# Kernel tuning notes

Hardware: AMD Instinct MI355X
Metric: run time of the kernel (lower is better)

The kernel has to match this reference:

```python
import jax, jax.numpy as jnp
import numpy as np

N_NODES, N_EDGES, N_FEAT, N_HID = 50000, 800000, 512, 64


def gcn_conv(x, W, b, src, dst, ew):
    """PyG-style GCNConv: linear -> symmetric-normalized aggregation with self-loops -> +bias."""
    N = x.shape[0]
    h = x @ W  # [N, H]
    # degree includes the implicit self-loop of weight 1 (PyG gcn_norm default)
    deg = jax.ops.segment_sum(ew, dst, num_segments=N) + 1.0
    dinv = jax.lax.rsqrt(deg)  # deg^{-1/2}
    coef = dinv[src] * ew * dinv[dst]  # [E]
    out = jax.ops.segment_sum(h[src] * coef[:, None], dst, num_segments=N)
    out = out + h * (dinv * dinv)[:, None]  # self-loop contribution
    return out + b


def setup_inputs() -> dict:
    key = jax.random.key(0)
    k0, k1, k2, k3 = jax.random.split(key, 4)
    x = jax.random.normal(k0, (N_NODES, N_FEAT), dtype=jnp.float32)
    edge_index = jax.random.randint(k1, (2, N_EDGES), 0, N_NODES, dtype=jnp.int64)
    edge_weight = jnp.ones((N_EDGES,), dtype=jnp.float32)
    W1 = jax.random.normal(k2, (N_FEAT, N_HID), dtype=jnp.float32) * (1.0 / np.sqrt(N_FEAT))
    b1 = jnp.zeros((N_HID,), dtype=jnp.float32)
    W2 = jax.random.normal(k3, (N_HID, N_HID), dtype=jnp.float32) * (1.0 / np.sqrt(N_HID))
    b2 = jnp.zeros((N_HID,), dtype=jnp.float32)
    return {"x": x, "edge_index": edge_index, "edge_weight": edge_weight,
            "W1": W1, "b1": b1, "W2": W2, "b2": b2}


def reference(x, edge_index, edge_weight, W1, b1, W2, b2):
    # Grace.forward -> GCN_body.forward in eval mode (no dropout, no LN)
    src, dst = edge_index[0], edge_index[1]
    h = jax.nn.relu(gcn_conv(x, W1, b1, src, dst, edge_weight))
    h = jax.nn.relu(gcn_conv(h, W2, b2, src, dst, edge_weight))
    return h
```

## Files before the change

kernel.cpp:

```cpp
#include <hip/hip_runtime.h>
#include <hip/hip_bf16.h>

typedef __bf16 bf16x8 __attribute__((ext_vector_type(8)));
typedef float  f32x4  __attribute__((ext_vector_type(4)));

#define RNODES 64
#define ROWCAP 1792
#define NB 128
#define MAXNR 1024

__device__ __forceinline__ float bf_lo(unsigned int v) { return __uint_as_float(v << 16); }
__device__ __forceinline__ float bf_hi(unsigned int v) { return __uint_as_float(v & 0xFFFF0000u); }

__global__ void probe_kernel(const unsigned int* __restrict__ ew_raw,
                             const unsigned int* __restrict__ ei_raw,
                             int* __restrict__ flags) {
    if (blockIdx.x == 0 && threadIdx.x == 0) {
        flags[0] = (ew_raw[0] == 0x3F803F80u) ? 1 : 0;
        flags[1] = ((ei_raw[1] | ei_raw[3] | ei_raw[5] | ei_raw[7]) == 0u) ? 1 : 0;
        flags[2] = 0;
        flags[3] = 0;
        flags[4] = 1;
    }
}

__global__ void ones_kernel(const unsigned int* __restrict__ ew_raw,
                            int* __restrict__ flags, int E) {
    int f16 = flags[0];
    int nw = f16 ? (E >> 1) : E;
    unsigned int expect = f16 ? 0x3F803F80u : 0x3F800000u;
    int base = blockIdx.x * 1024 + threadIdx.x;
    unsigned int bad = 0;
    #pragma unroll
    for (int k = 0; k < 4; ++k) {
        int i = base + k * 256;
        if (i < nw) bad |= (ew_raw[i] ^ expect);
    }
    if (bad) flags[4] = 0;
}

__global__ void pack_kernel(const void* __restrict__ W, const int* __restrict__ flags,
                            __hip_bfloat16* __restrict__ Wp, int K) {
    int t = blockIdx.x * blockDim.x + threadIdx.x;
    if (t >= K * 64) return;
    int j  = t & 7;
    int l  = (t >> 3) & 63;
    int nt = (t >> 9) & 3;
    int kt = t >> 11;
    int k = kt * 32 + (l >> 4) * 8 + j;
    int n = nt * 16 + (l & 15);
    size_t gi = (size_t)k * 64 + n;
    if (flags[0]) Wp[t] = ((const __hip_bfloat16*)W)[gi];
    else          Wp[t] = __float2bfloat16(((const float*)W)[gi]);
}

__device__ __forceinline__ void gemm_body(const void* __restrict__ A,
                                          const __hip_bfloat16* __restrict__ Wp,
                                          int a_f32, __hip_bfloat16* __restrict__ out,
                                          int M, int K, int gt) {
    int wid  = gt >> 6;
    int lane = gt & 63;
    if (wid >= (M >> 4)) return;
    int row0 = wid << 4;
    int quad = lane >> 4, mr = lane & 15;

    const bf16x8* bp = (const bf16x8*)((const void*)Wp) + lane;

    f32x4 acc[4];
    #pragma unroll
    for (int nt = 0; nt < 4; ++nt) acc[nt] = (f32x4){0.f, 0.f, 0.f, 0.f};

    int KT = K >> 5;
    const __hip_bfloat16* ab   = (const __hip_bfloat16*)A + (size_t)(row0 + mr) * K + quad * 8;
    const float*          af32 = (const float*)A + (size_t)(row0 + mr) * K + quad * 8;

    for (int kt = 0; kt < KT; ++kt) {
        bf16x8 af;
        if (a_f32) {
            const float* ar = af32 + kt * 32;
            #pragma unroll
            for (int j = 0; j < 8; ++j) af[j] = (__bf16)ar[j];
        } else {
            af = ((const bf16x8*)((const void*)(ab + kt * 32)))[0];
        }
        #pragma unroll
        for (int nt = 0; nt < 4; ++nt) {
            bf16x8 bf = bp[(kt * 4 + nt) * 64];
            acc[nt] = __builtin_amdgcn_mfma_f32_16x16x32_bf16(af, bf, acc[nt], 0, 0, 0);
        }
    }

    __hip_bfloat16* o = out + (size_t)row0 * 64;
    #pragma unroll
    for (int nt = 0; nt < 4; ++nt)
        #pragma unroll
        for (int r = 0; r < 4; ++r)
            o[(size_t)(quad * 4 + r) * 64 + nt * 16 + mr] = __float2bfloat16(acc[nt][r]);
}

__global__ void gemm_mfma(const void* __restrict__ A, const __hip_bfloat16* __restrict__ Wp,
                          const int* __restrict__ flags, __hip_bfloat16* __restrict__ out,
                          int M, int K, int a_mode) {
    int gt = blockIdx.x * blockDim.x + threadIdx.x;
    int a_f32 = (a_mode == 2) && (flags[0] == 0);
    gemm_body(A, Wp, a_f32, out, M, K, gt);
}

__global__ void p1_kernel(const int* __restrict__ ei, const void* __restrict__ ew,
                          const int* __restrict__ flags,
                          int* __restrict__ blockhist, unsigned int* __restrict__ pkstage,
                          float* __restrict__ wstage, int E, int NR) {
    __shared__ int hist[MAXNR];
    int b = blockIdx.x, tid = threadIdx.x;
    for (int i = tid; i < NR; i += 256) hist[i] = 0;
    __syncthreads();
    int chunk = (E + NB - 1) / NB;
    int e0 = b * chunk;
    int e1 = e0 + chunk; if (e1 > E) e1 = E;
    int f16 = flags[0], i64 = flags[1], ones = flags[4];
    for (int e = e0 + tid; e < e1; e += 256) {
        int s, d;
        if (i64) { s = ei[2LL * e]; d = ei[2LL * ((long long)E + e)]; }
        else     { s = ei[e];       d = ei[E + e]; }
        int r = d >> 6;
        atomicAdd(&hist[r], 1);
        pkstage[e] = ((unsigned int)r << 22) | ((unsigned int)s << 6) | (unsigned int)(d & 63);
        if (!ones) {
            float w = f16 ? __bfloat162float(((const __hip_bfloat16*)ew)[e])
                          : ((const float*)ew)[e];
            wstage[e] = w;
        }
    }
    __syncthreads();
    for (int i = tid; i < NR; i += 256) blockhist[b * NR + i] = hist[i];
}

__global__ void p2_kernel(int* __restrict__ blockhist, int* __restrict__ rtot, int NR) {
    int r = blockIdx.x * blockDim.x + threadIdx.x;
    if (r >= NR) return;
    int run = r * ROWCAP;
    #pragma unroll 4
    for (int b = 0; b < NB; ++b) {
        int c = blockhist[b * NR + r];
        blockhist[b * NR + r] = run;
        run += c;
    }
    int tot = run - r * ROWCAP;
    rtot[r] = tot > ROWCAP ? ROWCAP : tot;
}

__global__ void p3_kernel(const int* __restrict__ blockhist,
                          const unsigned int* __restrict__ pkstage,
                          const float* __restrict__ wstage, const int* __restrict__ flags,
                          unsigned int* __restrict__ sortedR, float* __restrict__ sortedRW,
                          int E, int NR) {
    __shared__ int loff[MAXNR];
    int b = blockIdx.x, tid = threadIdx.x;
    for (int i = tid; i < NR; i += 256) loff[i] = blockhist[b * NR + i];
    __syncthreads();
    int chunk = (E + NB - 1) / NB;
    int e0 = b * chunk;
    int e1 = e0 + chunk; if (e1 > E) e1 = E;
    int ones = flags[4];
    for (int e = e0 + tid; e < e1; e += 256) {
        unsigned int pk = pkstage[e];
        int r = (int)(pk >> 22);
        int pos = atomicAdd(&loff[r], 1);
        if (pos < (r + 1) * ROWCAP) {
            sortedR[pos] = pk;
            if (!ones) sortedRW[pos] = wstage[e];
        }
    }
}

__global__ void range_kernel(const unsigned int* __restrict__ sortedR,
                             const float* __restrict__ sortedRW,
                             const int* __restrict__ rtot, const int* __restrict__ flags,
                             int* __restrict__ cnt, float* __restrict__ dinv,
                             int* __restrict__ row_ptr,
                             int* __restrict__ sortedS, float* __restrict__ sortedW, int N) {
    __shared__ unsigned int sd[ROWCAP];
    __shared__ float sw[ROWCAP];
    __shared__ int   cnt0[RNODES], pref[RNODES], slot[RNODES];
    __shared__ float wsum[RNODES];

    int r   = blockIdx.x;
    int tid = threadIdx.x;
    int ones = flags[4];
    int T = rtot[r];

    if (tid < RNODES) { cnt0[tid] = 0; wsum[tid] = 0.f; }
    __syncthreads();

    size_t g = (size_t)r * ROWCAP;
    for (int t = tid; t < T; t += 256) {
        sd[t] = sortedR[g + t];
        if (!ones) sw[t] = sortedRW[g + t];
    }
    __syncthreads();

    for (int k = tid; k < T; k += 256) {
        int dl = sd[k] & (RNODES - 1);
        atomicAdd(&cnt0[dl], 1);
        if (!ones) atomicAdd(&wsum[dl], sw[k]);
    }
    __syncthreads();

    if (tid < RNODES) pref[tid] = cnt0[tid];
    __syncthreads();
    for (int off = 1; off < RNODES; off <<= 1) {
        int v = (tid < RNODES && tid >= off) ? pref[tid - off] : 0;
        __syncthreads();
        if (tid < RNODES) pref[tid] += v;
        __syncthreads();
    }
    if (tid < RNODES) {
        int excl = pref[tid] - cnt0[tid];
        int n = r * RNODES + tid;
        slot[tid] = r * ROWCAP + excl;
        if (n < N) {
            cnt[n]     = cnt0[tid];
            row_ptr[n] = r * ROWCAP + excl;
            float wd = ones ? (float)cnt0[tid] : wsum[tid];
            dinv[n]  = rsqrtf(wd + 1.0f);
        }
    }
    __syncthreads();

    for (int k = tid; k < T; k += 256) {
        unsigned int v = sd[k];
        int dl = v & (RNODES - 1);
        int p = atomicAdd(&slot[dl], 1);
        sortedS[p] = (int)((v >> 6) & 0xFFFFu);
        if (!ones) sortedW[p] = sw[k];
    }
}

__global__ void check_fast(const void* __restrict__ A, const void* __restrict__ W,
                           int* __restrict__ flags, const __hip_bfloat16* __restrict__ out,
                           int N, int K, int a_mode, int fidx) {
    __shared__ float xs[4 * 512];
    int f16 = flags[0];
    int a_f32 = (a_mode == 2) && (f16 == 0);
    int tid = threadIdx.x;
    int total = 4 * K;
    for (int t = tid; t < total; t += 256) {
        int nn = t / K, kk = t - nn * K;
        int n = (int)(((long long)(blockIdx.x * 4 + nn) * 977) % N);
        long long gi = (long long)n * K + kk;
        float v = a_f32 ? (float)(__bf16)(((const float*)A)[gi])
                        : __bfloat162float(((const __hip_bfloat16*)A)[gi]);
        xs[t] = v;
    }
    __syncthreads();
    int j = tid & 63, local = tid >> 6;
    int n = (int)(((long long)(blockIdx.x * 4 + local) * 977) % N);
    const float* xr = xs + local * K;
    float acc = 0.f;
    if (f16) {
        const __hip_bfloat16* Wb = (const __hip_bfloat16*)W;
        #pragma unroll 8
        for (int k = 0; k < K; ++k) acc += xr[k] * __bfloat162float(Wb[(long long)k * 64 + j]);
    } else {
        const float* Wf = (const float*)W;
        #pragma unroll 8
        for (int k = 0; k < K; ++k) acc += xr[k] * (float)(__bf16)(Wf[(long long)k * 64 + j]);
    }
    float d = __bfloat162float(out[(size_t)n * 64 + j]) - acc;
    if (!(fabsf(d) <= 0.05f)) atomicAdd(&flags[fidx], 1);
}

__global__ void gemm_fix(const void* __restrict__ A, const void* __restrict__ W,
                         const int* __restrict__ flags, __hip_bfloat16* __restrict__ out,
                         int N, int K, int a_mode, int fidx) {
    if (flags[fidx] == 0) return;
    __shared__ float xs[4 * 512];
    int node0 = blockIdx.x * 4;
    int tid = threadIdx.x;
    int f16 = flags[0];
    int a_f32 = (a_mode == 2) && (f16 == 0);
    int total = 4 * K;
    for (int t = tid; t < total; t += 256) {
        int nn = t / K, kk = t - nn * K;
        long long gi = (long long)(node0 + nn) * K + kk;
        float v = a_f32 ? ((const float*)A)[gi]
                        : __bfloat162float(((const __hip_bfloat16*)A)[gi]);
        xs[t] = v;
    }
    __syncthreads();
    int j = tid & 63, local = tid >> 6;
    int n = node0 + local;
    if (n >= N) return;
    const float* xr = xs + local * K;
    float acc = 0.f;
    if (f16) {
        const __hip_bfloat16* Wb = (const __hip_bfloat16*)W;
        #pragma unroll 8
        for (int k = 0; k < K; ++k) acc += xr[k] * __bfloat162float(Wb[(long long)k * 64 + j]);
    } else {
        const float* Wf = (const float*)W;
        #pragma unroll 8
        for (int k = 0; k < K; ++k) acc += xr[k] * Wf[(long long)k * 64 + j];
    }
    out[(long long)n * 64 + j] = __float2bfloat16(acc);
}

__global__ void gather_kernel(const __hip_bfloat16* __restrict__ h,
                              const int* __restrict__ sortedS, const float* __restrict__ sortedW,
                              const int* __restrict__ cnt, const int* __restrict__ row_ptr,
                              const float* __restrict__ dinv,
                              const void* __restrict__ bias, const int* __restrict__ flags,
                              void* __restrict__ out, int internal, int N) {
    int gt = blockIdx.x * blockDim.x + threadIdx.x;
    int n = gt >> 5, jl = gt & 31;
    if (n >= N) return;
    int f16 = flags[0], ones = flags[4];
    float dn = dinv[n];
    int deg = cnt[n];
    int base = row_ptr[n];
    const int*   p  = sortedS + base;
    const float* pw = sortedW + base;
    const unsigned int* h32 = (const unsigned int*)h;
    float a0 = 0.f, a1 = 0.f;
    int s = 0;
    for (; s + 4 <= deg; s += 4) {
        int s0 = p[s], s1 = p[s + 1], s2 = p[s + 2], s3 = p[s + 3];
        float c0 = dinv[s0] * dn, c1 = dinv[s1] * dn;
        float c2 = dinv[s2] * dn, c3 = dinv[s3] * dn;
        if (!ones) { c0 *= pw[s]; c1 *= pw[s + 1]; c2 *= pw[s + 2]; c3 *= pw[s + 3]; }
        unsigned int v0 = h32[(size_t)s0 * 32 + jl];
        unsigned int v1 = h32[(size_t)s1 * 32 + jl];
        unsigned int v2 = h32[(size_t)s2 * 32 + jl];
        unsigned int v3 = h32[(size_t)s3 * 32 + jl];
        a0 += c0 * bf_lo(v0) + c1 * bf_lo(v1) + c2 * bf_lo(v2) + c3 * bf_lo(v3);
        a1 += c0 * bf_hi(v0) + c1 * bf_hi(v1) + c2 * bf_hi(v2) + c3 * bf_hi(v3);
    }
    for (; s < deg; ++s) {
        int s0 = p[s];
        float c = dinv[s0] * dn;
        if (!ones) c *= pw[s];
        unsigned int v = h32[(size_t)s0 * 32 + jl];
        a0 += c * bf_lo(v);
        a1 += c * bf_hi(v);
    }
    unsigned int vs = h32[(size_t)n * 32 + jl];
    float dn2 = dn * dn;
    a0 += dn2 * bf_lo(vs);
    a1 += dn2 * bf_hi(vs);
    if (f16) {
        unsigned int bv = ((const unsigned int*)bias)[jl];
        a0 += bf_lo(bv);
        a1 += bf_hi(bv);
    } else {
        a0 += ((const float*)bias)[jl * 2];
        a1 += ((const float*)bias)[jl * 2 + 1];
    }
    a0 = fmaxf(a0, 0.f);
    a1 = fmaxf(a1, 0.f);
    if (internal | f16) {
        __hip_bfloat16 b0 = __float2bfloat16(a0), b1 = __float2bfloat16(a1);
        unsigned int pack = ((unsigned int)(*(unsigned short*)&b1) << 16)
                          | (unsigned int)(*(unsigned short*)&b0);
        ((unsigned int*)out)[(size_t)n * 32 + jl] = pack;
    } else {
        ((float*)out)[(size_t)n * 64 + jl * 2]     = a0;
        ((float*)out)[(size_t)n * 64 + jl * 2 + 1] = a1;
    }
}

extern "C" void kernel_launch(void* const* d_in, const int* in_sizes, int n_in,
                              void* d_out, int out_size, void* d_ws, size_t ws_size,
                              hipStream_t stream) {
    const void* x  = d_in[0];
    const int*  ei = (const int*)d_in[1];
    const void* ew = d_in[2];
    const void* W1 = d_in[3];
    const void* b1 = d_in[4];
    const void* W2 = d_in[5];
    const void* b2 = d_in[6];

    const int H = in_sizes[4];
    const int F = in_sizes[3] / H;
    const int N = in_sizes[0] / F;
    const int E = in_sizes[1] / 2;

    const int NR = (N + RNODES - 1) / RNODES;

    char* w = (char*)d_ws;
    size_t off = 0;
    auto alloc = [&](size_t bytes) {
        char* r = w + off;
        off += (bytes + 255) & ~(size_t)255;
        return r;
    };
    int*   flags     = (int*)alloc(32);
    int*   blockhist = (int*)alloc((size_t)NB * NR * 4);
    int*   rtot      = (int*)alloc((size_t)NR * 4);
    int*   cnt       = (int*)alloc((size_t)N * 4);
    float* dinv      = (float*)alloc((size_t)N * 4);
    int*   row_ptr   = (int*)alloc((size_t)N * 4);
    unsigned int* pkstage = (unsigned int*)alloc((size_t)E * 4);
    float* wstage    = (float*)alloc((size_t)E * 4);
    unsigned int* sortedR = (unsigned int*)alloc((size_t)NR * ROWCAP * 4);
    float* sortedRW  = (float*)alloc((size_t)NR * ROWCAP * 4);
    int*   sortedS   = (int*)alloc((size_t)NR * ROWCAP * 4);
    float* sortedW   = (float*)alloc((size_t)NR * ROWCAP * 4);
    __hip_bfloat16* bufH = (__hip_bfloat16*)alloc((size_t)N * 64 * 2);
    __hip_bfloat16* bufR = (__hip_bfloat16*)alloc((size_t)N * 64 * 2);
    __hip_bfloat16* W1p  = (__hip_bfloat16*)alloc((size_t)F * 64 * 2);
    __hip_bfloat16* W2p  = (__hip_bfloat16*)alloc((size_t)H * 64 * 2);

    probe_kernel<<<1, 64, 0, stream>>>((const unsigned int*)ew, (const unsigned int*)ei, flags);
    ones_kernel<<<(E + 1023) / 1024, 256, 0, stream>>>((const unsigned int*)ew, flags, E);
    pack_kernel<<<(F * 64 + 255) / 256, 256, 0, stream>>>(W1, flags, W1p, F);
    pack_kernel<<<(H * 64 + 255) / 256, 256, 0, stream>>>(W2, flags, W2p, H);

    int gblocks = ((N / 16) * 64 + 255) / 256;

    p1_kernel<<<NB, 256, 0, stream>>>(ei, ew, flags, blockhist, pkstage, wstage, E, NR);
    p2_kernel<<<(NR + 255) / 256, 256, 0, stream>>>(blockhist, rtot, NR);
    p3_kernel<<<NB, 256, 0, stream>>>(blockhist, pkstage, wstage, flags,
                                      sortedR, sortedRW, E, NR);

    gemm_mfma<<<gblocks, 256, 0, stream>>>(x, W1p, flags, bufH, N, F, 2);

    range_kernel<<<NR, 256, 0, stream>>>(sortedR, sortedRW, rtot, flags,
                                         cnt, dinv, row_ptr, sortedS, sortedW, N);

    check_fast<<<64, 256, 0, stream>>>(x, W1, flags, bufH, N, F, 2, 2);
    gemm_fix<<<(N + 3) / 4, 256, 0, stream>>>(x, W1, flags, bufH, N, F, 2, 2);

    gather_kernel<<<(N * 32 + 255) / 256, 256, 0, stream>>>(bufH, sortedS, sortedW,
                                                            cnt, row_ptr, dinv,
                                                            b1, flags, bufR, 1, N);
    gemm_mfma<<<gblocks, 256, 0, stream>>>(bufR, W2p, flags, bufH, N, H, 0);
    check_fast<<<64, 256, 0, stream>>>(bufR, W2, flags, bufH, N, H, 0, 3);
    gemm_fix<<<(N + 3) / 4, 256, 0, stream>>>(bufR, W2, flags, bufH, N, H, 0, 3);
    gather_kernel<<<(N * 32 + 255) / 256, 256, 0, stream>>>(bufH, sortedS, sortedW,
                                                            cnt, row_ptr, dinv,
                                                            b2, flags, d_out, 0, N);
}
```

Baseline: 349.2 us.

## Co-schedule GEMM with edge binning and merge setup, check and fix launches

Probe and weight-pack are merged into one setup kernel. The first dense GEMM shares a launch with the edge histogram pass, which now also does the all-ones edge-weight scan. The prefix-sum pass shares a launch with the sampled GEMM check, and the scatter pass shares one with the fallback fix. The fix kernel becomes grid-stride over 256 blocks instead of one block per 4 nodes, so the usual early exit costs far fewer blocks. The aim is fewer launches and idle gaps, and overlapping GEMM work with the sort stages; in exchange the staged edge weights are now always written, because the all-ones result is not yet known at that point.

```diff
diff --git a/kernel.cpp b/kernel.cpp
--- a/kernel.cpp
+++ b/kernel.cpp
@@ -8,41 +8,13 @@
 #define ROWCAP 1792
 #define NB 128
 #define MAXNR 1024
+#define FIXB 256
 
 __device__ __forceinline__ float bf_lo(unsigned int v) { return __uint_as_float(v << 16); }
 __device__ __forceinline__ float bf_hi(unsigned int v) { return __uint_as_float(v & 0xFFFF0000u); }
 
-__global__ void probe_kernel(const unsigned int* __restrict__ ew_raw,
-                             const unsigned int* __restrict__ ei_raw,
-                             int* __restrict__ flags) {
-    if (blockIdx.x == 0 && threadIdx.x == 0) {
-        flags[0] = (ew_raw[0] == 0x3F803F80u) ? 1 : 0;
-        flags[1] = ((ei_raw[1] | ei_raw[3] | ei_raw[5] | ei_raw[7]) == 0u) ? 1 : 0;
-        flags[2] = 0;
-        flags[3] = 0;
-        flags[4] = 1;
-    }
-}
-
-__global__ void ones_kernel(const unsigned int* __restrict__ ew_raw,
-                            int* __restrict__ flags, int E) {
-    int f16 = flags[0];
-    int nw = f16 ? (E >> 1) : E;
-    unsigned int expect = f16 ? 0x3F803F80u : 0x3F800000u;
-    int base = blockIdx.x * 1024 + threadIdx.x;
-    unsigned int bad = 0;
-    #pragma unroll
-    for (int k = 0; k < 4; ++k) {
-        int i = base + k * 256;
-        if (i < nw) bad |= (ew_raw[i] ^ expect);
-    }
-    if (bad) flags[4] = 0;
-}
-
-__global__ void pack_kernel(const void* __restrict__ W, const int* __restrict__ flags,
-                            __hip_bfloat16* __restrict__ Wp, int K) {
-    int t = blockIdx.x * blockDim.x + threadIdx.x;
-    if (t >= K * 64) return;
+__device__ __forceinline__ void pack_one(const void* __restrict__ W, int f16,
+                                         __hip_bfloat16* __restrict__ Wp, int K, int t) {
     int j  = t & 7;
     int l  = (t >> 3) & 63;
     int nt = (t >> 9) & 3;
@@ -50,8 +22,27 @@
     int k = kt * 32 + (l >> 4) * 8 + j;
     int n = nt * 16 + (l & 15);
     size_t gi = (size_t)k * 64 + n;
-    if (flags[0]) Wp[t] = ((const __hip_bfloat16*)W)[gi];
-    else          Wp[t] = __float2bfloat16(((const float*)W)[gi]);
+    Wp[t] = f16 ? ((const __hip_bfloat16*)W)[gi]
+                : __float2bfloat16(((const float*)W)[gi]);
+}
+
+__global__ void setup_kernel(const unsigned int* __restrict__ ew_raw,
+                             const unsigned int* __restrict__ ei_raw,
+                             const void* __restrict__ W1, const void* __restrict__ W2,
+                             int* __restrict__ flags,
+                             __hip_bfloat16* __restrict__ W1p, __hip_bfloat16* __restrict__ W2p,
+                             int F, int H) {
+    int f16 = (ew_raw[0] == 0x3F803F80u) ? 1 : 0;
+    if (blockIdx.x == 0 && threadIdx.x == 0) {
+        flags[0] = f16;
+        flags[1] = ((ei_raw[1] | ei_raw[3] | ei_raw[5] | ei_raw[7]) == 0u) ? 1 : 0;
+        flags[2] = 0;
+        flags[3] = 0;
+        flags[4] = 1;
+    }
+    int t = blockIdx.x * 256 + threadIdx.x;
+    if (t < F * 64)            pack_one(W1, f16, W1p, F, t);
+    else if (t < (F + H) * 64) pack_one(W2, f16, W2p, H, t - F * 64);
 }
 
 __device__ __forceinline__ void gemm_body(const void* __restrict__ A,
@@ -106,18 +97,35 @@
     gemm_body(A, Wp, a_f32, out, M, K, gt);
 }
 
-__global__ void p1_kernel(const int* __restrict__ ei, const void* __restrict__ ew,
-                          const int* __restrict__ flags,
-                          int* __restrict__ blockhist, unsigned int* __restrict__ pkstage,
-                          float* __restrict__ wstage, int E, int NR) {
+__global__ void bgp1_kernel(const void* __restrict__ A, const __hip_bfloat16* __restrict__ Wp,
+                            __hip_bfloat16* __restrict__ outH,
+                            const int* __restrict__ ei, const void* __restrict__ ew,
+                            int* __restrict__ flags,
+                            int* __restrict__ blockhist, unsigned int* __restrict__ pkstage,
+                            float* __restrict__ wstage,
+                            int M, int K, int E, int NR, int gblocks) {
+    if ((int)blockIdx.x < gblocks) {
+        int gt = blockIdx.x * 256 + threadIdx.x;
+        gemm_body(A, Wp, flags[0] == 0, outH, M, K, gt);
+        return;
+    }
     __shared__ int hist[MAXNR];
-    int b = blockIdx.x, tid = threadIdx.x;
+    int b = blockIdx.x - gblocks, tid = threadIdx.x;
     for (int i = tid; i < NR; i += 256) hist[i] = 0;
     __syncthreads();
+    int f16 = flags[0], i64 = flags[1];
+
+    int nw = f16 ? (E >> 1) : E;
+    unsigned int expect = f16 ? 0x3F803F80u : 0x3F800000u;
+    int wchunk = (nw + NB - 1) / NB;
+    int w0 = b * wchunk, w1 = w0 + wchunk; if (w1 > nw) w1 = nw;
+    const unsigned int* ewr = (const unsigned int*)ew;
+    unsigned int bad = 0;
+    for (int i = w0 + tid; i < w1; i += 256) bad |= (ewr[i] ^ expect);
+    if (bad) flags[4] = 0;
+
     int chunk = (E + NB - 1) / NB;
-    int e0 = b * chunk;
-    int e1 = e0 + chunk; if (e1 > E) e1 = E;
-    int f16 = flags[0], i64 = flags[1], ones = flags[4];
+    int e0 = b * chunk, e1 = e0 + chunk; if (e1 > E) e1 = E;
     for (int e = e0 + tid; e < e1; e += 256) {
         int s, d;
         if (i64) { s = ei[2LL * e]; d = ei[2LL * ((long long)E + e)]; }
@@ -125,51 +133,137 @@
         int r = d >> 6;
         atomicAdd(&hist[r], 1);
         pkstage[e] = ((unsigned int)r << 22) | ((unsigned int)s << 6) | (unsigned int)(d & 63);
-        if (!ones) {
-            float w = f16 ? __bfloat162float(((const __hip_bfloat16*)ew)[e])
-                          : ((const float*)ew)[e];
-            wstage[e] = w;
-        }
+        wstage[e] = f16 ? __bfloat162float(((const __hip_bfloat16*)ew)[e])
+                        : ((const float*)ew)[e];
     }
     __syncthreads();
     for (int i = tid; i < NR; i += 256) blockhist[b * NR + i] = hist[i];
 }
 
-__global__ void p2_kernel(int* __restrict__ blockhist, int* __restrict__ rtot, int NR) {
-    int r = blockIdx.x * blockDim.x + threadIdx.x;
-    if (r >= NR) return;
-    int run = r * ROWCAP;
-    #pragma unroll 4
-    for (int b = 0; b < NB; ++b) {
-        int c = blockhist[b * NR + r];
-        blockhist[b * NR + r] = run;
-        run += c;
-    }
-    int tot = run - r * ROWCAP;
-    rtot[r] = tot > ROWCAP ? ROWCAP : tot;
-}
-
-__global__ void p3_kernel(const int* __restrict__ blockhist,
-                          const unsigned int* __restrict__ pkstage,
-                          const float* __restrict__ wstage, const int* __restrict__ flags,
-                          unsigned int* __restrict__ sortedR, float* __restrict__ sortedRW,
-                          int E, int NR) {
-    __shared__ int loff[MAXNR];
-    int b = blockIdx.x, tid = threadIdx.x;
-    for (int i = tid; i < NR; i += 256) loff[i] = blockhist[b * NR + i];
-    __syncthreads();
-    int chunk = (E + NB - 1) / NB;
-    int e0 = b * chunk;
-    int e1 = e0 + chunk; if (e1 > E) e1 = E;
-    int ones = flags[4];
-    for (int e = e0 + tid; e < e1; e += 256) {
-        unsigned int pk = pkstage[e];
-        int r = (int)(pk >> 22);
-        int pos = atomicAdd(&loff[r], 1);
-        if (pos < (r + 1) * ROWCAP) {
-            sortedR[pos] = pk;
-            if (!ones) sortedRW[pos] = wstage[e];
-        }
+__device__ __forceinline__ void check_body(const void* __restrict__ A, const void* __restrict__ W,
+                                           int* __restrict__ flags,
+                                           const __hip_bfloat16* __restrict__ out,
+                                           int N, int K, int a_mode, int fidx, int bid) {
+    __shared__ float xs[4 * 512];
+    int f16 = flags[0];
+    int a_f32 = (a_mode == 2) && (f16 == 0);
+    int tid = threadIdx.x;
+    int total = 4 * K;
+    for (int t = tid; t < total; t += 256) {
+        int nn = t / K, kk = t - nn * K;
+        int n = (int)(((long long)(bid * 4 + nn) * 977) % N);
+        long long gi = (long long)n * K + kk;
+        float v = a_f32 ? (float)(__bf16)(((const float*)A)[gi])
+                        : __bfloat162float(((const __hip_bfloat16*)A)[gi]);
+        xs[t] = v;
+    }
+    __syncthreads();
+    int j = tid & 63, local = tid >> 6;
+    int n = (int)(((long long)(bid * 4 + local) * 977) % N);
+    const float* xr = xs + local * K;
+    float acc = 0.f;
+    if (f16) {
+        const __hip_bfloat16* Wb = (const __hip_bfloat16*)W;
+        #pragma unroll 8
+        for (int k = 0; k < K; ++k) acc += xr[k] * __bfloat162float(Wb[(long long)k * 64 + j]);
+    } else {
+        const float* Wf = (const float*)W;
+        #pragma unroll 8
+        for (int k = 0; k < K; ++k) acc += xr[k] * (float)(__bf16)(Wf[(long long)k * 64 + j]);
+    }
+    float d = __bfloat162float(out[(size_t)n * 64 + j]) - acc;
+    if (!(fabsf(d) <= 0.05f)) atomicAdd(&flags[fidx], 1);
+}
+
+__device__ __forceinline__ void fix_body(const void* __restrict__ A, const void* __restrict__ W,
+                                         const int* __restrict__ flags,
+                                         __hip_bfloat16* __restrict__ out,
+                                         int N, int K, int a_mode, int fidx,
+                                         int bid, int nblocks) {
+    if (flags[fidx] == 0) return;
+    __shared__ float xs[4 * 512];
+    int tid = threadIdx.x;
+    int f16 = flags[0];
+    int a_f32 = (a_mode == 2) && (f16 == 0);
+    int total = 4 * K;
+    for (int node0 = bid * 4; node0 < N; node0 += nblocks * 4) {
+        __syncthreads();
+        for (int t = tid; t < total; t += 256) {
+            int nn = t / K, kk = t - nn * K;
+            if (node0 + nn < N) {
+                long long gi = (long long)(node0 + nn) * K + kk;
+                xs[t] = a_f32 ? ((const float*)A)[gi]
+                              : __bfloat162float(((const __hip_bfloat16*)A)[gi]);
+            }
+        }
+        __syncthreads();
+        int j = tid & 63, local = tid >> 6;
+        int n = node0 + local;
+        if (n < N) {
+            const float* xr = xs + local * K;
+            float acc = 0.f;
+            if (f16) {
+                const __hip_bfloat16* Wb = (const __hip_bfloat16*)W;
+                #pragma unroll 8
+                for (int k = 0; k < K; ++k) acc += xr[k] * __bfloat162float(Wb[(long long)k * 64 + j]);
+            } else {
+                const float* Wf = (const float*)W;
+                #pragma unroll 8
+                for (int k = 0; k < K; ++k) acc += xr[k] * Wf[(long long)k * 64 + j];
+            }
+            out[(long long)n * 64 + j] = __float2bfloat16(acc);
+        }
+    }
+}
+
+__global__ void p2chk_kernel(int* __restrict__ blockhist, int* __restrict__ rtot, int NR,
+                             const void* __restrict__ A, const void* __restrict__ W,
+                             int* __restrict__ flags, const __hip_bfloat16* __restrict__ out,
+                             int N, int K, int a_mode, int fidx, int p2b) {
+    if ((int)blockIdx.x < p2b) {
+        int r = blockIdx.x * 256 + threadIdx.x;
+        if (r >= NR) return;
+        int run = r * ROWCAP;
+        #pragma unroll 4
+        for (int b = 0; b < NB; ++b) {
+            int c = blockhist[b * NR + r];
+            blockhist[b * NR + r] = run;
+            run += c;
+        }
+        int tot = run - r * ROWCAP;
+        rtot[r] = tot > ROWCAP ? ROWCAP : tot;
+    } else {
+        check_body(A, W, flags, out, N, K, a_mode, fidx, blockIdx.x - p2b);
+    }
+}
+
+__global__ void p3fix_kernel(const int* __restrict__ blockhist,
+                             const unsigned int* __restrict__ pkstage,
+                             const float* __restrict__ wstage, const int* __restrict__ flags,
+                             unsigned int* __restrict__ sortedR, float* __restrict__ sortedRW,
+                             int E, int NR,
+                             const void* __restrict__ A, const void* __restrict__ W,
+                             __hip_bfloat16* __restrict__ out,
+                             int N, int K, int a_mode, int fidx) {
+    if ((int)blockIdx.x < NB) {
+        __shared__ int loff[MAXNR];
+        int b = blockIdx.x, tid = threadIdx.x;
+        for (int i = tid; i < NR; i += 256) loff[i] = blockhist[b * NR + i];
+        __syncthreads();
+        int chunk = (E + NB - 1) / NB;
+        int e0 = b * chunk, e1 = e0 + chunk; if (e1 > E) e1 = E;
+        int ones = flags[4];
+        for (int e = e0 + tid; e < e1; e += 256) {
+            unsigned int pk = pkstage[e];
+            int r = (int)(pk >> 22);
+            int pos = atomicAdd(&loff[r], 1);
+            if (pos < (r + 1) * ROWCAP) {
+                sortedR[pos] = pk;
+                if (!ones) sortedRW[pos] = wstage[e];
+            }
+        }
+    } else {
+        fix_body(A, W, flags, out, N, K, a_mode, fidx, blockIdx.x - NB, FIXB);
     }
 }
 
@@ -239,70 +333,13 @@
 __global__ void check_fast(const void* __restrict__ A, const void* __restrict__ W,
                            int* __restrict__ flags, const __hip_bfloat16* __restrict__ out,
                            int N, int K, int a_mode, int fidx) {
-    __shared__ float xs[4 * 512];
-    int f16 = flags[0];
-    int a_f32 = (a_mode == 2) && (f16 == 0);
-    int tid = threadIdx.x;
-    int total = 4 * K;
-    for (int t = tid; t < total; t += 256) {
-        int nn = t / K, kk = t - nn * K;
-        int n = (int)(((long long)(blockIdx.x * 4 + nn) * 977) % N);
-        long long gi = (long long)n * K + kk;
-        float v = a_f32 ? (float)(__bf16)(((const float*)A)[gi])
-                        : __bfloat162float(((const __hip_bfloat16*)A)[gi]);
-        xs[t] = v;
-    }
-    __syncthreads();
-    int j = tid & 63, local = tid >> 6;
-    int n = (int)(((long long)(blockIdx.x * 4 + local) * 977) % N);
-    const float* xr = xs + local * K;
-    float acc = 0.f;
-    if (f16) {
-        const __hip_bfloat16* Wb = (const __hip_bfloat16*)W;
-        #pragma unroll 8
-        for (int k = 0; k < K; ++k) acc += xr[k] * __bfloat162float(Wb[(long long)k * 64 + j]);
-    } else {
-        const float* Wf = (const float*)W;
-        #pragma unroll 8
-        for (int k = 0; k < K; ++k) acc += xr[k] * (float)(__bf16)(Wf[(long long)k * 64 + j]);
-    }
-    float d = __bfloat162float(out[(size_t)n * 64 + j]) - acc;
-    if (!(fabsf(d) <= 0.05f)) atomicAdd(&flags[fidx], 1);
+    check_body(A, W, flags, out, N, K, a_mode, fidx, blockIdx.x);
 }
 
 __global__ void gemm_fix(const void* __restrict__ A, const void* __restrict__ W,
                          const int* __restrict__ flags, __hip_bfloat16* __restrict__ out,
                          int N, int K, int a_mode, int fidx) {
-    if (flags[fidx] == 0) return;
-    __shared__ float xs[4 * 512];
-    int node0 = blockIdx.x * 4;
-    int tid = threadIdx.x;
-    int f16 = flags[0];
-    int a_f32 = (a_mode == 2) && (f16 == 0);
-    int total = 4 * K;
-    for (int t = tid; t < total; t += 256) {
-        int nn = t / K, kk = t - nn * K;
-        long long gi = (long long)(node0 + nn) * K + kk;
-        float v = a_f32 ? ((const float*)A)[gi]
-                        : __bfloat162float(((const __hip_bfloat16*)A)[gi]);
-        xs[t] = v;
-    }
-    __syncthreads();
-    int j = tid & 63, local = tid >> 6;
-    int n = node0 + local;
-    if (n >= N) return;
-    const float* xr = xs + local * K;
-    float acc = 0.f;
-    if (f16) {
-        const __hip_bfloat16* Wb = (const __hip_bfloat16*)W;
-        #pragma unroll 8
-        for (int k = 0; k < K; ++k) acc += xr[k] * __bfloat162float(Wb[(long long)k * 64 + j]);
-    } else {
-        const float* Wf = (const float*)W;
-        #pragma unroll 8
-        for (int k = 0; k < K; ++k) acc += xr[k] * Wf[(long long)k * 64 + j];
-    }
-    out[(long long)n * 64 + j] = __float2bfloat16(acc);
+    fix_body(A, W, flags, out, N, K, a_mode, fidx, blockIdx.x, FIXB);
 }
 
 __global__ void gather_kernel(const __hip_bfloat16* __restrict__ h,
@@ -410,32 +447,33 @@
     __hip_bfloat16* W1p  = (__hip_bfloat16*)alloc((size_t)F * 64 * 2);
     __hip_bfloat16* W2p  = (__hip_bfloat16*)alloc((size_t)H * 64 * 2);
 
-    probe_kernel<<<1, 64, 0, stream>>>((const unsigned int*)ew, (const unsigned int*)ei, flags);
-    ones_kernel<<<(E + 1023) / 1024, 256, 0, stream>>>((const unsigned int*)ew, flags, E);
-    pack_kernel<<<(F * 64 + 255) / 256, 256, 0, stream>>>(W1, flags, W1p, F);
-    pack_kernel<<<(H * 64 + 255) / 256, 256, 0, stream>>>(W2, flags, W2p, H);
-
     int gblocks = ((N / 16) * 64 + 255) / 256;
-
-    p1_kernel<<<NB, 256, 0, stream>>>(ei, ew, flags, blockhist, pkstage, wstage, E, NR);
-    p2_kernel<<<(NR + 255) / 256, 256, 0, stream>>>(blockhist, rtot, NR);
-    p3_kernel<<<NB, 256, 0, stream>>>(blockhist, pkstage, wstage, flags,
-                                      sortedR, sortedRW, E, NR);
-
-    gemm_mfma<<<gblocks, 256, 0, stream>>>(x, W1p, flags, bufH, N, F, 2);
+    int p2b = (NR + 255) / 256;
+
+    setup_kernel<<<((F + H) * 64 + 255) / 256, 256, 0, stream>>>(
+        (const unsigned int*)ew, (const unsigned int*)ei, W1, W2, flags, W1p, W2p, F, H);
+
+    bgp1_kernel<<<gblocks + NB, 256, 0, stream>>>(x, W1p, bufH, ei, ew, flags,
+                                                  blockhist, pkstage, wstage,
+                                                  N, F, E, NR, gblocks);
+
+    p2chk_kernel<<<p2b + 64, 256, 0, stream>>>(blockhist, rtot, NR,
+                                               x, W1, flags, bufH, N, F, 2, 2, p2b);
+
+    p3fix_kernel<<<NB + FIXB, 256, 0, stream>>>(blockhist, pkstage, wstage, flags,
+                                                sortedR, sortedRW, E, NR,
+                                                x, W1, bufH, N, F, 2, 2);
 
     range_kernel<<<NR, 256, 0, stream>>>(sortedR, sortedRW, rtot, flags,
                                          cnt, dinv, row_ptr, sortedS, sortedW, N);
-
-    check_fast<<<64, 256, 0, stream>>>(x, W1, flags, bufH, N, F, 2, 2);
-    gemm_fix<<<(N + 3) / 4, 256, 0, stream>>>(x, W1, flags, bufH, N, F, 2, 2);
 
     gather_kernel<<<(N * 32 + 255) / 256, 256, 0, stream>>>(bufH, sortedS, sortedW,
                                                             cnt, row_ptr, dinv,
                                                             b1, flags, bufR, 1, N);
     gemm_mfma<<<gblocks, 256, 0, stream>>>(bufR, W2p, flags, bufH, N, H, 0);
     check_fast<<<64, 256, 0, stream>>>(bufR, W2, flags, bufH, N, H, 0, 3);
-    gemm_fix<<<(N + 3) / 4, 256, 0, stream>>>(bufR, W2, flags, bufH, N, H, 0, 3);
+    gemm_fix<<<FIXB, 256, 0, stream>>>(bufR, W2, flags, bufH, N, H, 0, 3);
+
     gather_kernel<<<(N * 32 + 255) / 256, 256, 0, stream>>>(bufH, sortedS, sortedW,
                                                             cnt, row_ptr, dinv,
                                                             b2, flags, d_out, 0, N);
```

Result: faster. 308.7 us (-11.6%).
